# Optimization experiments

Hardware: AMD Instinct MI355X
Metric: run time of the kernel (lower is better)

Reference implementation:

```python
import jax, jax.numpy as jnp
import numpy as np

EMB = 512          # embedding_size
N_REL = 1000       # n_relation_type
BATCH = 131072
OFFSET = 1.0
EPS = 1e-12        # torch F.normalize clamp


def _l2_normalize(v):
    n = jnp.sqrt(jnp.sum(v * v, axis=-1, keepdims=True))
    return v / jnp.maximum(n, EPS)


def setup_inputs() -> dict:
    key = jax.random.key(0)
    k1, k2, k3, k4 = jax.random.split(key, 4)
    head_emb = jax.random.normal(k1, (BATCH, 2 * EMB), dtype=jnp.float32)
    tail_emb = jax.random.normal(k2, (BATCH, 2 * EMB), dtype=jnp.float32)
    relation_embedding = jax.random.normal(k3, (N_REL, EMB), dtype=jnp.float32) * 0.1
    relation_id = jax.random.randint(k4, (BATCH,), 0, N_REL)
    return {
        "head_emb": head_emb,
        "tail_emb": tail_emb,
        "relation_embedding": relation_embedding,
        "relation_id": relation_id,
    }


def reference(head_emb, tail_emb, relation_embedding, relation_id):
    # InterHT.score_triple (the module's forward)
    rel = relation_embedding[relation_id]                 # (B, E)
    head_main, head_aux = jnp.split(head_emb, 2, axis=-1)  # (B, E) each
    tail_main, tail_aux = jnp.split(tail_emb, 2, axis=-1)
    # normalize_entities=True -> L2-normalize all four parts
    head_main = _l2_normalize(head_main)
    tail_main = _l2_normalize(tail_main)
    head_aux = _l2_normalize(head_aux)
    tail_aux = _l2_normalize(tail_aux)
    d = head_main * (tail_aux + OFFSET) + rel - tail_main * (head_aux + OFFSET)
    # scoring_norm p=2 reduction along embedding dim, negated
    return -jnp.sqrt(jnp.sum(d * d, axis=-1))             # (B,)
```

## Files before the change

### kernel.cpp

```cpp
#include <hip/hip_runtime.h>


constexpr int EMB = 512;

typedef float fvec4 __attribute__((ext_vector_type(4)));

__device__ __forceinline__ float dot4(const fvec4 v) {
    return v.x * v.x + v.y * v.y + v.z * v.z + v.w * v.w;
}

__device__ __forceinline__ float wave_allreduce(float v) {
#pragma unroll
    for (int off = 32; off >= 1; off >>= 1)
        v += __shfl_xor(v, off, 64);
    return v;
}

__global__ __launch_bounds__(256) void interht_score_kernel(
    const float* __restrict__ head,
    const float* __restrict__ tail,
    const float* __restrict__ rel_emb,
    const int* __restrict__ rel_id,
    float* __restrict__ out,
    int batch)
{
    const int lane = threadIdx.x & 63;
    const int wave = threadIdx.x >> 6;
    const int row  = (blockIdx.x << 2) + wave;
    if (row >= batch) return;

    const fvec4* h = reinterpret_cast<const fvec4*>(head) + (size_t)row * (2 * EMB / 4);
    const fvec4* t = reinterpret_cast<const fvec4*>(tail) + (size_t)row * (2 * EMB / 4);

    fvec4 hm0 = __builtin_nontemporal_load(&h[lane]);
    fvec4 hm1 = __builtin_nontemporal_load(&h[64 + lane]);
    fvec4 ha0 = __builtin_nontemporal_load(&h[128 + lane]);
    fvec4 ha1 = __builtin_nontemporal_load(&h[192 + lane]);
    fvec4 tm0 = __builtin_nontemporal_load(&t[lane]);
    fvec4 tm1 = __builtin_nontemporal_load(&t[64 + lane]);
    fvec4 ta0 = __builtin_nontemporal_load(&t[128 + lane]);
    fvec4 ta1 = __builtin_nontemporal_load(&t[192 + lane]);

    const int rid = rel_id[row];
    const fvec4* r = reinterpret_cast<const fvec4*>(rel_emb) + (size_t)rid * (EMB / 4);
    fvec4 r0 = r[lane];
    fvec4 r1 = r[64 + lane];

    const float s_hm = wave_allreduce(dot4(hm0) + dot4(hm1));
    const float s_ha = wave_allreduce(dot4(ha0) + dot4(ha1));
    const float s_tm = wave_allreduce(dot4(tm0) + dot4(tm1));
    const float s_ta = wave_allreduce(dot4(ta0) + dot4(ta1));

    const float i_hm = 1.0f / fmaxf(sqrtf(s_hm), 1e-12f);
    const float i_ha = 1.0f / fmaxf(sqrtf(s_ha), 1e-12f);
    const float i_tm = 1.0f / fmaxf(sqrtf(s_tm), 1e-12f);
    const float i_ta = 1.0f / fmaxf(sqrtf(s_ta), 1e-12f);

    float acc = 0.0f;
    auto accum = [&](float hm, float ha, float tm, float ta, float rr) {
        const float d = hm * i_hm * (ta * i_ta + 1.0f) + rr
                      - tm * i_tm * (ha * i_ha + 1.0f);
        acc = fmaf(d, d, acc);
    };
    accum(hm0.x, ha0.x, tm0.x, ta0.x, r0.x);
    accum(hm0.y, ha0.y, tm0.y, ta0.y, r0.y);
    accum(hm0.z, ha0.z, tm0.z, ta0.z, r0.z);
    accum(hm0.w, ha0.w, tm0.w, ta0.w, r0.w);
    accum(hm1.x, ha1.x, tm1.x, ta1.x, r1.x);
    accum(hm1.y, ha1.y, tm1.y, ta1.y, r1.y);
    accum(hm1.z, ha1.z, tm1.z, ta1.z, r1.z);
    accum(hm1.w, ha1.w, tm1.w, ta1.w, r1.w);

    acc = wave_allreduce(acc);
    if (lane == 0) out[row] = -sqrtf(acc);
}

extern "C" void kernel_launch(void* const* d_in, const int* in_sizes, int n_in,
                              void* d_out, int out_size, void* d_ws, size_t ws_size,
                              hipStream_t stream) {
    const float* head    = (const float*)d_in[0];
    const float* tail    = (const float*)d_in[1];
    const float* rel_emb = (const float*)d_in[2];
    const int*   rel_id  = (const int*)d_in[3];
    float* out = (float*)d_out;

    const int batch = in_sizes[3];
    const int rows_per_block = 4;
    const int grid = (batch + rows_per_block - 1) / rows_per_block;

    interht_score_kernel<<<grid, 256, 0, stream>>>(head, tail, rel_emb, rel_id,
                                                   out, batch);
}
```

Before: 917.1 us.

## Process multiple rows per wave with software-prefetched next-row loads

Each wave now handles a chunk of 8 consecutive rows and issues the loads for the next row before reducing the current one, double-buffering rows in registers. The aim is to hide global memory latency on a bandwidth-bound streaming kernel and to amortize block launch cost. It also adds launch bounds with a minimum of 4 blocks per CU and a nontemporal output store. The price is higher register pressure, and an 8x smaller grid that may reduce the number of outstanding requests.

```diff
diff --git a/kernel.cpp b/kernel.cpp
--- a/kernel.cpp
+++ b/kernel.cpp
@@ -2,6 +2,7 @@
 
 
 constexpr int EMB = 512;
+constexpr int CHUNK = 8;
 
 typedef float fvec4 __attribute__((ext_vector_type(4)));
 
@@ -16,40 +17,31 @@
     return v;
 }
 
-__global__ __launch_bounds__(256) void interht_score_kernel(
-    const float* __restrict__ head,
-    const float* __restrict__ tail,
-    const float* __restrict__ rel_emb,
-    const int* __restrict__ rel_id,
-    float* __restrict__ out,
-    int batch)
-{
-    const int lane = threadIdx.x & 63;
-    const int wave = threadIdx.x >> 6;
-    const int row  = (blockIdx.x << 2) + wave;
-    if (row >= batch) return;
+struct Row {
+    fvec4 hm0, hm1, ha0, ha1, tm0, tm1, ta0, ta1;
+};
 
+__device__ __forceinline__ void load_row(const float* __restrict__ head,
+                                         const float* __restrict__ tail,
+                                         int row, int lane, Row& R) {
     const fvec4* h = reinterpret_cast<const fvec4*>(head) + (size_t)row * (2 * EMB / 4);
     const fvec4* t = reinterpret_cast<const fvec4*>(tail) + (size_t)row * (2 * EMB / 4);
+    R.hm0 = __builtin_nontemporal_load(&h[lane]);
+    R.hm1 = __builtin_nontemporal_load(&h[64 + lane]);
+    R.ha0 = __builtin_nontemporal_load(&h[128 + lane]);
+    R.ha1 = __builtin_nontemporal_load(&h[192 + lane]);
+    R.tm0 = __builtin_nontemporal_load(&t[lane]);
+    R.tm1 = __builtin_nontemporal_load(&t[64 + lane]);
+    R.ta0 = __builtin_nontemporal_load(&t[128 + lane]);
+    R.ta1 = __builtin_nontemporal_load(&t[192 + lane]);
+}
 
-    fvec4 hm0 = __builtin_nontemporal_load(&h[lane]);
-    fvec4 hm1 = __builtin_nontemporal_load(&h[64 + lane]);
-    fvec4 ha0 = __builtin_nontemporal_load(&h[128 + lane]);
-    fvec4 ha1 = __builtin_nontemporal_load(&h[192 + lane]);
-    fvec4 tm0 = __builtin_nontemporal_load(&t[lane]);
-    fvec4 tm1 = __builtin_nontemporal_load(&t[64 + lane]);
-    fvec4 ta0 = __builtin_nontemporal_load(&t[128 + lane]);
-    fvec4 ta1 = __builtin_nontemporal_load(&t[192 + lane]);
-
-    const int rid = rel_id[row];
-    const fvec4* r = reinterpret_cast<const fvec4*>(rel_emb) + (size_t)rid * (EMB / 4);
-    fvec4 r0 = r[lane];
-    fvec4 r1 = r[64 + lane];
-
-    const float s_hm = wave_allreduce(dot4(hm0) + dot4(hm1));
-    const float s_ha = wave_allreduce(dot4(ha0) + dot4(ha1));
-    const float s_tm = wave_allreduce(dot4(tm0) + dot4(tm1));
-    const float s_ta = wave_allreduce(dot4(ta0) + dot4(ta1));
+__device__ __forceinline__ void process_row(const Row& R, const fvec4 r0, const fvec4 r1,
+                                            int lane, int row, float* __restrict__ out) {
+    const float s_hm = wave_allreduce(dot4(R.hm0) + dot4(R.hm1));
+    const float s_ha = wave_allreduce(dot4(R.ha0) + dot4(R.ha1));
+    const float s_tm = wave_allreduce(dot4(R.tm0) + dot4(R.tm1));
+    const float s_ta = wave_allreduce(dot4(R.ta0) + dot4(R.ta1));
 
     const float i_hm = 1.0f / fmaxf(sqrtf(s_hm), 1e-12f);
     const float i_ha = 1.0f / fmaxf(sqrtf(s_ha), 1e-12f);
@@ -62,17 +54,59 @@
                       - tm * i_tm * (ha * i_ha + 1.0f);
         acc = fmaf(d, d, acc);
     };
-    accum(hm0.x, ha0.x, tm0.x, ta0.x, r0.x);
-    accum(hm0.y, ha0.y, tm0.y, ta0.y, r0.y);
-    accum(hm0.z, ha0.z, tm0.z, ta0.z, r0.z);
-    accum(hm0.w, ha0.w, tm0.w, ta0.w, r0.w);
-    accum(hm1.x, ha1.x, tm1.x, ta1.x, r1.x);
-    accum(hm1.y, ha1.y, tm1.y, ta1.y, r1.y);
-    accum(hm1.z, ha1.z, tm1.z, ta1.z, r1.z);
-    accum(hm1.w, ha1.w, tm1.w, ta1.w, r1.w);
+    accum(R.hm0.x, R.ha0.x, R.tm0.x, R.ta0.x, r0.x);
+    accum(R.hm0.y, R.ha0.y, R.tm0.y, R.ta0.y, r0.y);
+    accum(R.hm0.z, R.ha0.z, R.tm0.z, R.ta0.z, r0.z);
+    accum(R.hm0.w, R.ha0.w, R.tm0.w, R.ta0.w, r0.w);
+    accum(R.hm1.x, R.ha1.x, R.tm1.x, R.ta1.x, r1.x);
+    accum(R.hm1.y, R.ha1.y, R.tm1.y, R.ta1.y, r1.y);
+    accum(R.hm1.z, R.ha1.z, R.tm1.z, R.ta1.z, r1.z);
+    accum(R.hm1.w, R.ha1.w, R.tm1.w, R.ta1.w, r1.w);
 
     acc = wave_allreduce(acc);
-    if (lane == 0) out[row] = -sqrtf(acc);
+    if (lane == 0) __builtin_nontemporal_store(-sqrtf(acc), &out[row]);
+}
+
+__global__ __launch_bounds__(256, 4) void interht_score_kernel(
+    const float* __restrict__ head,
+    const float* __restrict__ tail,
+    const float* __restrict__ rel_emb,
+    const int* __restrict__ rel_id,
+    float* __restrict__ out,
+    int batch)
+{
+    const int lane = threadIdx.x & 63;
+    const int wave = threadIdx.x >> 6;
+    const int gw   = (blockIdx.x << 2) + wave;
+
+    int row = gw * CHUNK;
+    const int row_end = min(row + CHUNK, batch);
+    if (row >= row_end) return;
+
+    Row cur, nxt;
+    int rid_cur = rel_id[row];
+    load_row(head, tail, row, lane, cur);
+
+#pragma unroll 2
+    for (; row < row_end; ) {
+        const fvec4* r = reinterpret_cast<const fvec4*>(rel_emb)
+                       + (size_t)rid_cur * (EMB / 4);
+        const fvec4 r0 = r[lane];
+        const fvec4 r1 = r[64 + lane];
+
+        const int nrow = row + 1;
+        int rid_nxt = 0;
+        if (nrow < row_end) {
+            rid_nxt = rel_id[nrow];
+            load_row(head, tail, nrow, lane, nxt);
+        }
+
+        process_row(cur, r0, r1, lane, row, out);
+
+        cur = nxt;
+        rid_cur = rid_nxt;
+        row = nrow;
+    }
 }
 
 extern "C" void kernel_launch(void* const* d_in, const int* in_sizes, int n_in,
@@ -85,7 +119,7 @@
     float* out = (float*)d_out;
 
     const int batch = in_sizes[3];
-    const int rows_per_block = 4;
+    const int rows_per_block = 4 * CHUNK;
     const int grid = (batch + rows_per_block - 1) / rows_per_block;
 
     interht_score_kernel<<<grid, 256, 0, stream>>>(head, tail, rel_emb, rel_id,
```

Result: slower. 937.5 us (+2.2%).
